# Kernel tuning notes

Hardware: AMD Instinct MI355X
Metric: run time of the kernel (lower is better)

The kernel has to match this reference:

```python
import jax, jax.numpy as jnp
import numpy as np

LN_EPS = 1e-5


def setup_inputs() -> dict:
    key = jax.random.key(0)
    kx, kA, kB, kC, kg = jax.random.split(key, 5)
    B, S, D, N = 16, 1024, 1024, 64
    x = jax.random.uniform(kx, (B, S, D), dtype=jnp.float32)
    A = jax.random.uniform(kA, (D, N), dtype=jnp.float32)          # torch.rand init
    W_B = jax.random.normal(kB, (N, D), dtype=jnp.float32) * 0.02  # B: d_model -> d_state
    W_C = jax.random.normal(kC, (D, N), dtype=jnp.float32) * 0.02  # C.weight_raw, [d_model, d_state]
    gamma = jax.random.normal(kg, (D,), dtype=jnp.float32) * 0.1   # TopologicalNorm scale (sigmoid-bounded)
    return {"x": x, "A": A, "W_B": W_B, "W_C": W_C, "gamma": gamma}


def reference(x, A, W_B, W_C, gamma):
    # x: [B, S, D]
    Bb, S, D = x.shape
    N = A.shape[1]
    A_sig = jax.nn.sigmoid(A)          # [D, N] state decay gates
    Bw = jax.nn.sigmoid(W_B)           # [N, D] sigmoid-constrained input projection
    Cw = jax.nn.sigmoid(W_C)           # [D, N] sigmoid-constrained readout weights
    g = jax.nn.sigmoid(gamma)          # [D]   bounded norm scale

    def step(h, x_t):
        # x_t: [B, D], h: [B, D, N]
        b_t = x_t @ Bw.T                                             # [B, N]
        inp = b_t[:, None, :] * x_t[:, :, None]                      # [B, D, N] outer product morphism
        h = jnp.clip(h * A_sig[None] + inp, 0.0, 1.0)                # clamped state update
        y = jnp.sum(h * Cw[None], axis=-1)                           # [B, D] weighted readout
        mu = jnp.mean(y, axis=-1, keepdims=True)
        var = jnp.var(y, axis=-1, keepdims=True)
        y = (y - mu) * jax.lax.rsqrt(var + LN_EPS) * g               # TopologicalNorm
        return h, y

    h0 = jnp.zeros((Bb, D, N), dtype=x.dtype)
    _, ys = jax.lax.scan(step, h0, jnp.swapaxes(x, 0, 1))            # ys: [S, B, D]
    y = jnp.swapaxes(ys, 0, 1)                                       # [B, S, D]
    return jnp.clip(y + x, 0.0, 1.0)
```

## Files before the change

### kernel.cpp

```cpp
#include <hip/hip_runtime.h>
#include <math.h>

#define D_MODEL 1024
#define N_STATE 64
#define BATCH   16
#define SEQ     1024
#define CS      16
#define SEGLEN  512
#define WARM    64
#define SAT_T   1.0001f
#define LPS     20

__device__ __forceinline__ float sigmoidf_dev(float v) {
    return 1.0f / (1.0f + expf(-v));
}

template<int CTRL>
__device__ __forceinline__ float dpp_add(float v) {
    int s = __builtin_amdgcn_update_dpp(0, __float_as_int(v), CTRL, 0xF, 0xF, true);
    return v + __int_as_float(s);
}

template<int CTRL>
__device__ __forceinline__ float dpp_min(float v) {
    int s = __builtin_amdgcn_update_dpp(0, __float_as_int(v), CTRL, 0xF, 0xF, true);
    return fminf(v, __int_as_float(s));
}

#define CLAMP01(v) __builtin_amdgcn_fmed3f((v), 0.0f, 1.0f)

__global__ __launch_bounds__(256) void k0_precompute(
        const float* __restrict__ A, const float* __restrict__ W_B,
        const float* __restrict__ W_C, const float* __restrict__ gamma,
        float* __restrict__ A_sig, float* __restrict__ BwT,
        float* __restrict__ Cs, float* __restrict__ gs) {
    int i = blockIdx.x * 256 + threadIdx.x;
    if (i < D_MODEL * N_STATE) {
        A_sig[i] = sigmoidf_dev(A[i]);
        Cs[i]    = sigmoidf_dev(W_C[i]);
        int d = i >> 6, n = i & 63;
        BwT[i] = sigmoidf_dev(W_B[n * D_MODEL + d]);
        if (i < D_MODEL) gs[i] = sigmoidf_dev(gamma[i]);
    }
}

__global__ __launch_bounds__(256) void k0b_csum(
        const float* __restrict__ Cs, float* __restrict__ csum) {
    int d = blockIdx.x * 256 + threadIdx.x;
    if (d >= D_MODEL) return;
    const float4* c = (const float4*)(Cs + (size_t)d * N_STATE);
    float w[16];
#pragma unroll
    for (int q = 0; q < 16; ++q) {
        float4 v = c[q];
        w[q] = (v.x + v.y) + (v.z + v.w);
    }
#pragma unroll
    for (int off = 1; off < 16; off <<= 1) {
        float tmp[16];
#pragma unroll
        for (int q = 0; q < 16; ++q) tmp[q] = w[q] + w[q ^ off];
#pragma unroll
        for (int q = 0; q < 16; ++q) w[q] = tmp[q];
    }
    csum[d] = w[0];
}

__global__ __launch_bounds__(256) void k1_bt_gemm(
        const float* __restrict__ x, const float* __restrict__ BwT,
        float* __restrict__ bt, float* __restrict__ btmin) {
    __shared__ float xs[2][16][68];
    __shared__ float bs[2][16][64];

    const int t  = threadIdx.x;
    const int r  = t >> 4;
    const int c  = t & 15;
    const int m0 = blockIdx.x * 64;

    const int sm  = t >> 2;
    const int sk4 = (t & 3) * 4;

    float acc[4][4];
#pragma unroll
    for (int i = 0; i < 4; ++i)
#pragma unroll
        for (int j = 0; j < 4; ++j) acc[i][j] = 0.0f;

    {
        float4 xv = *(const float4*)(x + (size_t)(m0 + sm) * D_MODEL + sk4);
        float4 bv = *(const float4*)(BwT + t * 4);
        xs[0][sk4 + 0][sm] = xv.x;
        xs[0][sk4 + 1][sm] = xv.y;
        xs[0][sk4 + 2][sm] = xv.z;
        xs[0][sk4 + 3][sm] = xv.w;
        *(float4*)(&bs[0][0][0] + t * 4) = bv;
    }
    __syncthreads();

    for (int kt = 0; kt < 64; ++kt) {
        const int p = kt & 1;
        const bool more = (kt + 1 < 64);
        float4 xv, bv;
        if (more) {
            const int k0 = (kt + 1) * 16;
            xv = *(const float4*)(x + (size_t)(m0 + sm) * D_MODEL + k0 + sk4);
            bv = *(const float4*)(BwT + (size_t)k0 * N_STATE + t * 4);
        }

#pragma unroll
        for (int kk = 0; kk < 16; ++kk) {
            const float4 ap = *(const float4*)(&xs[p][kk][r * 4]);
            const float4 bq = *(const float4*)(&bs[p][kk][c * 4]);
            acc[0][0] = fmaf(ap.x, bq.x, acc[0][0]);
            acc[0][1] = fmaf(ap.x, bq.y, acc[0][1]);
            acc[0][2] = fmaf(ap.x, bq.z, acc[0][2]);
            acc[0][3] = fmaf(ap.x, bq.w, acc[0][3]);
            acc[1][0] = fmaf(ap.y, bq.x, acc[1][0]);
            acc[1][1] = fmaf(ap.y, bq.y, acc[1][1]);
            acc[1][2] = fmaf(ap.y, bq.z, acc[1][2]);
            acc[1][3] = fmaf(ap.y, bq.w, acc[1][3]);
            acc[2][0] = fmaf(ap.z, bq.x, acc[2][0]);
            acc[2][1] = fmaf(ap.z, bq.y, acc[2][1]);
            acc[2][2] = fmaf(ap.z, bq.z, acc[2][2]);
            acc[2][3] = fmaf(ap.z, bq.w, acc[2][3]);
            acc[3][0] = fmaf(ap.w, bq.x, acc[3][0]);
            acc[3][1] = fmaf(ap.w, bq.y, acc[3][1]);
            acc[3][2] = fmaf(ap.w, bq.z, acc[3][2]);
            acc[3][3] = fmaf(ap.w, bq.w, acc[3][3]);
        }

        if (more) {
            const int q = 1 - p;
            xs[q][sk4 + 0][sm] = xv.x;
            xs[q][sk4 + 1][sm] = xv.y;
            xs[q][sk4 + 2][sm] = xv.z;
            xs[q][sk4 + 3][sm] = xv.w;
            *(float4*)(&bs[q][0][0] + t * 4) = bv;
        }
        __syncthreads();
    }

#pragma unroll
    for (int i = 0; i < 4; ++i) {
        *(float4*)(&bt[(size_t)(m0 + r * 4 + i) * N_STATE + c * 4]) =
            make_float4(acc[i][0], acc[i][1], acc[i][2], acc[i][3]);
        float bm = fminf(fminf(acc[i][0], acc[i][1]), fminf(acc[i][2], acc[i][3]));
        bm = dpp_min<0xB1>(bm);  bm = dpp_min<0x4E>(bm);
        bm = dpp_min<0x141>(bm); bm = dpp_min<0x140>(bm);
        if (c == 0) btmin[m0 + r * 4 + i] = bm;
    }
}

__global__ __launch_bounds__(256, 8) void k2_scan(
        const float* __restrict__ x, const float* __restrict__ bt,
        const float* __restrict__ btmin,
        const float* __restrict__ A_sig, const float* __restrict__ Cs,
        float* __restrict__ y_raw) {
    const int t    = threadIdx.x;
    const int lane = t & 63;
    const int wv   = t >> 6;
    const int nq   = lane & 15;
    const int cl   = wv * 4 + (lane >> 4);
    const int bid  = blockIdx.x;
    const int seg  = bid & 1;
    const int dg   = (bid >> 1) & 63;
    const int b    = bid >> 7;
    const int d0   = dg * 16;
    const int d    = d0 + cl;

    const int nWarm  = seg ? (WARM / CS) : 0;
    const int nTot   = nWarm + (SEGLEN / CS);
    const int sStart = seg * SEGLEN - nWarm * CS;

    __shared__ __align__(16) float lbt [2][CS * 64];
    __shared__ __align__(16) float lx  [2][CS * 16];
    __shared__ __align__(16) float lpxT[2][16 * LPS];

    const float4 av = *(const float4*)(A_sig + (size_t)d * N_STATE + nq * 4);
    const float4 cv = *(const float4*)(Cs    + (size_t)d * N_STATE + nq * 4);

    float h0 = 0.f, h1 = 0.f, h2 = 0.f, h3 = 0.f;

    const float* btp  = bt    + (size_t)b * SEQ * N_STATE + (size_t)sStart * N_STATE;
    const float* btmp = btmin + (size_t)b * SEQ + sStart;
    const float* xpp  = x + (size_t)b * SEQ * D_MODEL + (size_t)sStart * D_MODEL + d0;
    float* ystore = y_raw + (size_t)b * SEQ * D_MODEL + (size_t)seg * SEGLEN * D_MODEL + d;

    const int xst = t >> 4;
    const int xdd = t & 15;

    {
        float4 b4 = *(const float4*)(btp + t * 4);
        float  xv = xpp[(size_t)xst * D_MODEL + xdd];
        float  bm = fmaxf(btmp[xst], 0.f);
        *(float4*)(&lbt[0][t * 4]) = b4;
        lx[0][t] = xv;
        lpxT[0][xdd * LPS + xst] = xv * bm;
    }
    btp  += CS * N_STATE;
    btmp += CS;
    xpp  += (size_t)CS * D_MODEL;
    __syncthreads();

    for (int ch = 0; ch < nTot; ++ch) {
        const int p = ch & 1;
        float4 nb; float nx, npx;
        const bool more = (ch + 1 < nTot);
        if (more) {
            nb  = *(const float4*)(btp + t * 4);
            nx  = xpp[(size_t)xst * D_MODEL + xdd];
            npx = nx * fmaxf(btmp[xst], 0.f);
            btp  += CS * N_STATE;
            btmp += CS;
            xpp  += (size_t)CS * D_MODEL;
        }

        const float* Lb = lbt[p];
        const float* Lx = lx [p];
        const float* Lp = &lpxT[p][cl * LPS];

        if (ch < nWarm) {
#pragma unroll
            for (int g = 0; g < 4; ++g) {
                const float4 pq = *(const float4*)(Lp + g * 4);
                const float qmin = fminf(fminf(pq.x, pq.y), fminf(pq.z, pq.w));
                if (__all(qmin >= SAT_T)) { h0 = h1 = h2 = h3 = 1.f; continue; }
                const float pmv[4] = {pq.x, pq.y, pq.z, pq.w};
#pragma unroll
                for (int j = 0; j < 4; ++j) {
                    const int i = g * 4 + j;
                    const float pm = pmv[j];
                    if (__all(pm >= SAT_T)) { h0 = h1 = h2 = h3 = 1.f; continue; }
                    const float  xt = Lx[i * 16 + cl];
                    const float4 bv = *(const float4*)(Lb + i * 64 + nq * 4);
                    h0 = CLAMP01(fmaf(h0, av.x, bv.x * xt));
                    h1 = CLAMP01(fmaf(h1, av.y, bv.y * xt));
                    h2 = CLAMP01(fmaf(h2, av.z, bv.z * xt));
                    h3 = CLAMP01(fmaf(h3, av.w, bv.w * xt));
                }
            }
        } else {
#pragma unroll
            for (int g = 0; g < 4; ++g) {
                const float4 pq = *(const float4*)(Lp + g * 4);
                const float qmin = fminf(fminf(pq.x, pq.y), fminf(pq.z, pq.w));
                if (__all(qmin >= SAT_T)) { h0 = h1 = h2 = h3 = 1.f; continue; }
                const float pmv[4] = {pq.x, pq.y, pq.z, pq.w};
#pragma unroll
                for (int j = 0; j < 4; ++j) {
                    const int i = g * 4 + j;
                    const float pm = pmv[j];
                    if (__all(pm >= SAT_T)) { h0 = h1 = h2 = h3 = 1.f; continue; }
                    const float  xt = Lx[i * 16 + cl];
                    const float4 bv = *(const float4*)(Lb + i * 64 + nq * 4);
                    h0 = CLAMP01(fmaf(h0, av.x, bv.x * xt));
                    h1 = CLAMP01(fmaf(h1, av.y, bv.y * xt));
                    h2 = CLAMP01(fmaf(h2, av.z, bv.z * xt));
                    h3 = CLAMP01(fmaf(h3, av.w, bv.w * xt));
                    float y = fmaf(h0, cv.x, h1 * cv.y) + fmaf(h2, cv.z, h3 * cv.w);
                    y = dpp_add<0xB1>(y);
                    y = dpp_add<0x4E>(y);
                    y = dpp_add<0x141>(y);
                    y = dpp_add<0x140>(y);
                    if (nq == 0 && !(pm >= SAT_T)) ystore[(size_t)i * D_MODEL] = y;
                }
            }
            ystore += (size_t)CS * D_MODEL;
        }

        if (more) {
            const int q = 1 - p;
            *(float4*)(&lbt[q][t * 4]) = nb;
            lx[q][t] = nx;
            lpxT[q][xdd * LPS + xst] = npx;
        }
        __syncthreads();
    }
}

__global__ __launch_bounds__(256, 1) void k3_norm(
        const float* __restrict__ x, const float* __restrict__ gs,
        const float* __restrict__ btmin, const float* __restrict__ csum,
        float* __restrict__ y) {
    const int row = blockIdx.x;
    const int t   = threadIdx.x;
    const size_t base = (size_t)row * D_MODEL + t * 4;
    const float bm = fmaxf(btmin[row], 0.f);

    float4 xv  = *(const float4*)(x + base);
    float4 cs4 = *(const float4*)(csum + t * 4);
    const bool p0 = (xv.x * bm >= SAT_T);
    const bool p1 = (xv.y * bm >= SAT_T);
    const bool p2 = (xv.z * bm >= SAT_T);
    const bool p3 = (xv.w * bm >= SAT_T);
    float y0 = cs4.x, y1 = cs4.y, y2 = cs4.z, y3 = cs4.w;
    if (!(p0 && p1 && p2 && p3)) {
        float4 ld = *(const float4*)(y + base);
        if (!p0) y0 = ld.x;
        if (!p1) y1 = ld.y;
        if (!p2) y2 = ld.z;
        if (!p3) y3 = ld.w;
    }

    float s1 = (y0 + y1) + (y2 + y3);
#pragma unroll
    for (int off = 32; off > 0; off >>= 1) s1 += __shfl_xor(s1, off);

    __shared__ float red[8];
    const int w = t >> 6;
    if ((t & 63) == 0) red[w] = s1;
    __syncthreads();
    const float mu = (red[0] + red[1] + red[2] + red[3]) * (1.0f / (float)D_MODEL);

    const float dx0 = y0 - mu, dx1 = y1 - mu, dx2 = y2 - mu, dx3 = y3 - mu;
    float s2 = (dx0 * dx0 + dx1 * dx1) + (dx2 * dx2 + dx3 * dx3);
#pragma unroll
    for (int off = 32; off > 0; off >>= 1) s2 += __shfl_xor(s2, off);
    if ((t & 63) == 0) red[4 + w] = s2;
    __syncthreads();
    const float var = (red[4] + red[5] + red[6] + red[7]) * (1.0f / (float)D_MODEL);
    const float rs  = 1.0f / sqrtf(var + 1e-5f);

    float4 gv = *(const float4*)(gs + t * 4);
    float4 o;
    o.x = fminf(fmaxf(dx0 * rs * gv.x + xv.x, 0.f), 1.f);
    o.y = fminf(fmaxf(dx1 * rs * gv.y + xv.y, 0.f), 1.f);
    o.z = fminf(fmaxf(dx2 * rs * gv.z + xv.z, 0.f), 1.f);
    o.w = fminf(fmaxf(dx3 * rs * gv.w + xv.w, 0.f), 1.f);
    *(float4*)(y + base) = o;
}

extern "C" void kernel_launch(void* const* d_in, const int* in_sizes, int n_in,
                              void* d_out, int out_size, void* d_ws, size_t ws_size,
                              hipStream_t stream) {
    (void)in_sizes; (void)n_in; (void)out_size; (void)ws_size;
    const float* x     = (const float*)d_in[0];
    const float* A     = (const float*)d_in[1];
    const float* W_B   = (const float*)d_in[2];
    const float* W_C   = (const float*)d_in[3];
    const float* gamma = (const float*)d_in[4];
    float* out = (float*)d_out;
    float* ws  = (float*)d_ws;

    float* bt    = ws;
    float* A_sig = ws + 1048576;
    float* BwT   = ws + 1048576 + 65536;
    float* Cs    = ws + 1048576 + 2 * 65536;
    float* gs    = ws + 1048576 + 3 * 65536;
    float* btmin = ws + 1048576 + 3 * 65536 + 1024;
    float* csum  = ws + 1048576 + 3 * 65536 + 1024 + 16384;

    k0_precompute<<<dim3(256), dim3(256), 0, stream>>>(A, W_B, W_C, gamma,
                                                       A_sig, BwT, Cs, gs);
    k0b_csum<<<dim3(4), dim3(256), 0, stream>>>(Cs, csum);
    k1_bt_gemm<<<dim3(256), dim3(256), 0, stream>>>(x, BwT, bt, btmin);
    k2_scan<<<dim3(2048), dim3(256), 0, stream>>>(x, bt, btmin, A_sig, Cs, out);
    k3_norm<<<dim3(BATCH * SEQ), dim3(256), 0, stream>>>(x, gs, btmin, csum, out);
}
```

Measured before the change: 221.7 us.

## Fold csum into precompute kernel and split-K the bt GEMM across two groups

Merges the column-sum kernel into the precompute kernel by recomputing the sigmoid of W_C directly in extra blocks, which removes one kernel launch and its dependency. The bt GEMM now uses 512-thread blocks where two 256-thread groups each take half of the K dimension. Their partial sums are reduced through shared memory, doubling the waves per block and halving the serial K loop. The cost is extra LDS (including a 16KB reduction buffer), a final reduction step, and redundant sigmoid evaluation for csum.

Result: faster. 206.5 us (-6.9%).

```diff
diff --git a/kernel.cpp b/kernel.cpp
--- a/kernel.cpp
+++ b/kernel.cpp
@@ -33,52 +33,56 @@
         const float* __restrict__ A, const float* __restrict__ W_B,
         const float* __restrict__ W_C, const float* __restrict__ gamma,
         float* __restrict__ A_sig, float* __restrict__ BwT,
-        float* __restrict__ Cs, float* __restrict__ gs) {
-    int i = blockIdx.x * 256 + threadIdx.x;
-    if (i < D_MODEL * N_STATE) {
+        float* __restrict__ Cs, float* __restrict__ gs,
+        float* __restrict__ csum) {
+    const int bid = blockIdx.x;
+    const int t   = threadIdx.x;
+    if (bid < 256) {
+        int i = bid * 256 + t;
         A_sig[i] = sigmoidf_dev(A[i]);
         Cs[i]    = sigmoidf_dev(W_C[i]);
         int d = i >> 6, n = i & 63;
         BwT[i] = sigmoidf_dev(W_B[n * D_MODEL + d]);
         if (i < D_MODEL) gs[i] = sigmoidf_dev(gamma[i]);
-    }
-}
-
-__global__ __launch_bounds__(256) void k0b_csum(
-        const float* __restrict__ Cs, float* __restrict__ csum) {
-    int d = blockIdx.x * 256 + threadIdx.x;
-    if (d >= D_MODEL) return;
-    const float4* c = (const float4*)(Cs + (size_t)d * N_STATE);
-    float w[16];
-#pragma unroll
-    for (int q = 0; q < 16; ++q) {
-        float4 v = c[q];
-        w[q] = (v.x + v.y) + (v.z + v.w);
-    }
-#pragma unroll
-    for (int off = 1; off < 16; off <<= 1) {
-        float tmp[16];
-#pragma unroll
-        for (int q = 0; q < 16; ++q) tmp[q] = w[q] + w[q ^ off];
-#pragma unroll
-        for (int q = 0; q < 16; ++q) w[q] = tmp[q];
-    }
-    csum[d] = w[0];
-}
-
-__global__ __launch_bounds__(256) void k1_bt_gemm(
+    } else {
+        int d = (bid - 256) * 256 + t;
+        const float4* c = (const float4*)(W_C + (size_t)d * N_STATE);
+        float w[16];
+#pragma unroll
+        for (int q = 0; q < 16; ++q) {
+            float4 v = c[q];
+            w[q] = (sigmoidf_dev(v.x) + sigmoidf_dev(v.y)) +
+                   (sigmoidf_dev(v.z) + sigmoidf_dev(v.w));
+        }
+#pragma unroll
+        for (int off = 1; off < 16; off <<= 1) {
+            float tmp[16];
+#pragma unroll
+            for (int q = 0; q < 16; ++q) tmp[q] = w[q] + w[q ^ off];
+#pragma unroll
+            for (int q = 0; q < 16; ++q) w[q] = tmp[q];
+        }
+        csum[d] = w[0];
+    }
+}
+
+__global__ __launch_bounds__(512) void k1_bt_gemm(
         const float* __restrict__ x, const float* __restrict__ BwT,
         float* __restrict__ bt, float* __restrict__ btmin) {
-    __shared__ float xs[2][16][68];
-    __shared__ float bs[2][16][64];
-
-    const int t  = threadIdx.x;
-    const int r  = t >> 4;
-    const int c  = t & 15;
-    const int m0 = blockIdx.x * 64;
-
-    const int sm  = t >> 2;
-    const int sk4 = (t & 3) * 4;
+    __shared__ float xs[2][2][16][68];
+    __shared__ float bs[2][2][16][64];
+    __shared__ float accb[16][256];
+
+    const int t   = threadIdx.x;
+    const int g   = t >> 8;
+    const int tid = t & 255;
+    const int r   = tid >> 4;
+    const int c   = tid & 15;
+    const int m0  = blockIdx.x * 64;
+    const int kb  = g * 512;
+
+    const int sm  = tid >> 2;
+    const int sk4 = (tid & 3) * 4;
 
     float acc[4][4];
 #pragma unroll
@@ -87,30 +91,30 @@
         for (int j = 0; j < 4; ++j) acc[i][j] = 0.0f;
 
     {
-        float4 xv = *(const float4*)(x + (size_t)(m0 + sm) * D_MODEL + sk4);
-        float4 bv = *(const float4*)(BwT + t * 4);
-        xs[0][sk4 + 0][sm] = xv.x;
-        xs[0][sk4 + 1][sm] = xv.y;
-        xs[0][sk4 + 2][sm] = xv.z;
-        xs[0][sk4 + 3][sm] = xv.w;
-        *(float4*)(&bs[0][0][0] + t * 4) = bv;
-    }
-    __syncthreads();
-
-    for (int kt = 0; kt < 64; ++kt) {
+        float4 xv = *(const float4*)(x + (size_t)(m0 + sm) * D_MODEL + kb + sk4);
+        float4 bv = *(const float4*)(BwT + (size_t)kb * N_STATE + tid * 4);
+        xs[g][0][sk4 + 0][sm] = xv.x;
+        xs[g][0][sk4 + 1][sm] = xv.y;
+        xs[g][0][sk4 + 2][sm] = xv.z;
+        xs[g][0][sk4 + 3][sm] = xv.w;
+        *(float4*)(&bs[g][0][0][0] + tid * 4) = bv;
+    }
+    __syncthreads();
+
+    for (int kt = 0; kt < 32; ++kt) {
         const int p = kt & 1;
-        const bool more = (kt + 1 < 64);
+        const bool more = (kt + 1 < 32);
         float4 xv, bv;
         if (more) {
-            const int k0 = (kt + 1) * 16;
+            const int k0 = kb + (kt + 1) * 16;
             xv = *(const float4*)(x + (size_t)(m0 + sm) * D_MODEL + k0 + sk4);
-            bv = *(const float4*)(BwT + (size_t)k0 * N_STATE + t * 4);
+            bv = *(const float4*)(BwT + (size_t)k0 * N_STATE + tid * 4);
         }
 
 #pragma unroll
         for (int kk = 0; kk < 16; ++kk) {
-            const float4 ap = *(const float4*)(&xs[p][kk][r * 4]);
-            const float4 bq = *(const float4*)(&bs[p][kk][c * 4]);
+            const float4 ap = *(const float4*)(&xs[g][p][kk][r * 4]);
+            const float4 bq = *(const float4*)(&bs[g][p][kk][c * 4]);
             acc[0][0] = fmaf(ap.x, bq.x, acc[0][0]);
             acc[0][1] = fmaf(ap.x, bq.y, acc[0][1]);
             acc[0][2] = fmaf(ap.x, bq.z, acc[0][2]);
@@ -131,23 +135,37 @@
 
         if (more) {
             const int q = 1 - p;
-            xs[q][sk4 + 0][sm] = xv.x;
-            xs[q][sk4 + 1][sm] = xv.y;
-            xs[q][sk4 + 2][sm] = xv.z;
-            xs[q][sk4 + 3][sm] = xv.w;
-            *(float4*)(&bs[q][0][0] + t * 4) = bv;
+            xs[g][q][sk4 + 0][sm] = xv.x;
+            xs[g][q][sk4 + 1][sm] = xv.y;
+            xs[g][q][sk4 + 2][sm] = xv.z;
+            xs[g][q][sk4 + 3][sm] = xv.w;
+            *(float4*)(&bs[g][q][0][0] + tid * 4) = bv;
         }
         __syncthreads();
     }
 
-#pragma unroll
-    for (int i = 0; i < 4; ++i) {
-        *(float4*)(&bt[(size_t)(m0 + r * 4 + i) * N_STATE + c * 4]) =
-            make_float4(acc[i][0], acc[i][1], acc[i][2], acc[i][3]);
-        float bm = fminf(fminf(acc[i][0], acc[i][1]), fminf(acc[i][2], acc[i][3]));
-        bm = dpp_min<0xB1>(bm);  bm = dpp_min<0x4E>(bm);
-        bm = dpp_min<0x141>(bm); bm = dpp_min<0x140>(bm);
-        if (c == 0) btmin[m0 + r * 4 + i] = bm;
+    if (g == 1) {
+#pragma unroll
+        for (int i = 0; i < 4; ++i)
+#pragma unroll
+            for (int j = 0; j < 4; ++j)
+                accb[i * 4 + j][tid] = acc[i][j];
+    }
+    __syncthreads();
+    if (g == 0) {
+#pragma unroll
+        for (int i = 0; i < 4; ++i) {
+            float o0 = acc[i][0] + accb[i * 4 + 0][tid];
+            float o1 = acc[i][1] + accb[i * 4 + 1][tid];
+            float o2 = acc[i][2] + accb[i * 4 + 2][tid];
+            float o3 = acc[i][3] + accb[i * 4 + 3][tid];
+            *(float4*)(&bt[(size_t)(m0 + r * 4 + i) * N_STATE + c * 4]) =
+                make_float4(o0, o1, o2, o3);
+            float bm = fminf(fminf(o0, o1), fminf(o2, o3));
+            bm = dpp_min<0xB1>(bm);  bm = dpp_min<0x4E>(bm);
+            bm = dpp_min<0x141>(bm); bm = dpp_min<0x140>(bm);
+            if (c == 0) btmin[m0 + r * 4 + i] = bm;
+        }
     }
 }
 
@@ -350,10 +368,9 @@
     float* btmin = ws + 1048576 + 3 * 65536 + 1024;
     float* csum  = ws + 1048576 + 3 * 65536 + 1024 + 16384;
 
-    k0_precompute<<<dim3(256), dim3(256), 0, stream>>>(A, W_B, W_C, gamma,
-                                                       A_sig, BwT, Cs, gs);
-    k0b_csum<<<dim3(4), dim3(256), 0, stream>>>(Cs, csum);
-    k1_bt_gemm<<<dim3(256), dim3(256), 0, stream>>>(x, BwT, bt, btmin);
+    k0_precompute<<<dim3(260), dim3(256), 0, stream>>>(A, W_B, W_C, gamma,
+                                                       A_sig, BwT, Cs, gs, csum);
+    k1_bt_gemm<<<dim3(256), dim3(512), 0, stream>>>(x, BwT, bt, btmin);
     k2_scan<<<dim3(2048), dim3(256), 0, stream>>>(x, bt, btmin, A_sig, Cs, out);
     k3_norm<<<dim3(BATCH * SEQ), dim3(256), 0, stream>>>(x, gs, btmin, csum, out);
 }
```
